# Kernel optimization log

Hardware: AMD Instinct MI355X
Metric: run time of the kernel (lower is better)

The kernel has to match this reference:

```python
import jax, jax.numpy as jnp
import numpy as np

T, B, I, H, O, L = 512, 64, 256, 1024, 256, 3


def _gru_layer(x_seq, h0, w_ih, w_hh, b_ih, b_hh):
    """PyTorch-style GRU layer. x_seq: [T,B,Iin], h0: [B,H].
    Gate order in stacked weights is (r, z, n), matching torch.nn.GRU."""
    # Precompute all input-side gate projections with one big GEMM: [T,B,3H]
    gi = jnp.einsum('tbi,gi->tbg', x_seq, w_ih) + b_ih

    def step(h, gi_t):
        gh = h @ w_hh.T + b_hh                      # [B,3H]
        i_r, i_z, i_n = jnp.split(gi_t, 3, axis=-1)
        h_r, h_z, h_n = jnp.split(gh, 3, axis=-1)
        r = jax.nn.sigmoid(i_r + h_r)
        z = jax.nn.sigmoid(i_z + h_z)
        n = jnp.tanh(i_n + r * h_n)
        h_new = (1.0 - z) * n + z * h
        return h_new, h_new

    h_last, ys = jax.lax.scan(step, h0, gi)
    return ys, h_last


def setup_inputs() -> dict:
    key = jax.random.key(0)
    ks = jax.random.split(key, 16)
    s = 1.0 / np.sqrt(H)  # torch init scale ~ U(-1/sqrt(H), 1/sqrt(H))
    inp = {
        'x': jax.random.normal(ks[0], (T, B, I), jnp.float32),
        'h0': jax.random.normal(ks[1], (L, B, H), jnp.float32),
        'fc_w': jax.random.uniform(ks[2], (O, H), jnp.float32, -s, s),
        'fc_b': jax.random.uniform(ks[3], (O,), jnp.float32, -s, s),
    }
    k_idx = 4
    for l in range(L):
        iin = I if l == 0 else H
        inp[f'w_ih_l{l}'] = jax.random.uniform(ks[k_idx], (3 * H, iin), jnp.float32, -s, s)
        inp[f'w_hh_l{l}'] = jax.random.uniform(ks[k_idx + 1], (3 * H, H), jnp.float32, -s, s)
        inp[f'b_ih_l{l}'] = jax.random.uniform(ks[k_idx + 2], (3 * H,), jnp.float32, -s, s)
        inp[f'b_hh_l{l}'] = jax.random.uniform(ks[k_idx + 3], (3 * H,), jnp.float32, -s, s)
        k_idx += 4
    return inp


def reference(x, h0,
              w_ih_l0, w_hh_l0, b_ih_l0, b_hh_l0,
              w_ih_l1, w_hh_l1, b_ih_l1, b_hh_l1,
              w_ih_l2, w_hh_l2, b_ih_l2, b_hh_l2,
              fc_w, fc_b):
    layer_params = [
        (w_ih_l0, w_hh_l0, b_ih_l0, b_hh_l0),
        (w_ih_l1, w_hh_l1, b_ih_l1, b_hh_l1),
        (w_ih_l2, w_hh_l2, b_ih_l2, b_hh_l2),
    ]
    out = x
    h_lasts = []
    for l, (wi, wh, bi, bh) in enumerate(layer_params):
        out, h_l = _gru_layer(out, h0[l], wi, wh, bi, bh)
        h_lasts.append(h_l)
    y = out @ fc_w.T + fc_b        # [T,B,O]
    h_final = jnp.stack(h_lasts)   # [L,B,H]
    return y, h_final
```

## Files before the change

### kernel.cpp

```cpp
#include <hip/hip_runtime.h>
#include <cstdint>
#include <cstddef>

#define TT 512
#define BB 64
#define II 256
#define HH 1024
#define OO 256
#define LL 3
#define NBLK 192
#define TSLOTS 513
#define SSTEPS 520
#define LDS_GI   98304
#define GI_STRIDE 68
#define LDS_HT   (LDS_GI + 26112)
#define LDS_TOTAL (LDS_HT + 2048)

typedef _Float16 half8 __attribute__((ext_vector_type(8)));
typedef float floatx4 __attribute__((ext_vector_type(4)));
typedef float float4v __attribute__((ext_vector_type(4)));

__device__ __forceinline__ floatx4 mfma16(half8 a, half8 b, floatx4 c) {
    return __builtin_amdgcn_mfma_f32_16x16x32_f16(a, b, c, 0, 0, 0);
}

__device__ __forceinline__ float fast_sig(float x) {
    return __builtin_amdgcn_rcpf(1.f + __builtin_amdgcn_exp2f(-1.44269504f * x));
}
__device__ __forceinline__ float fast_tanh(float x) {
    return 1.f - 2.f * __builtin_amdgcn_rcpf(1.f + __builtin_amdgcn_exp2f(2.88539008f * x));
}

__global__ void cast_f32_f16(const float* __restrict__ in, _Float16* __restrict__ out, int n) {
    int i = blockIdx.x * 256 + threadIdx.x;
    if (i < n) out[i] = (_Float16)in[i];
}

__global__ void init_h(const float* __restrict__ h0, _Float16* __restrict__ hseq,
                       unsigned* __restrict__ flags) {
    int i = blockIdx.x * 256 + threadIdx.x;
    if (i < 256) flags[i] = 0u;
    if (i >= LL * BB * HH) return;
    int l = i / (BB * HH);
    int rest = i - l * (BB * HH);
    hseq[((size_t)l * TSLOTS) * BB * HH + rest] = (_Float16)h0[i];
}

__global__ void frag_reorder(const float* __restrict__ src, _Float16* __restrict__ dst,
                             int K, int nks) {
    int idx = blockIdx.x * 256 + threadIdx.x;
    int total = 64 * 3 * nks * 64;
    if (idx >= total) return;
    int lane = idx & 63;
    int r = idx >> 6;
    int ks = r % nks; r /= nks;
    int g = r % 3;
    int jb = r / 3;
    int row = g * HH + jb * 16 + (lane & 15);
    int col = ks * 32 + (lane >> 4) * 8;
    const float* s8 = src + (size_t)row * K + col;
    half8 v;
#pragma unroll
    for (int i = 0; i < 8; ++i) v[i] = (_Float16)s8[i];
    *(half8*)(dst + (size_t)idx * 8) = v;
}

struct PArgs {
    const float* x;
    const float* h0;
    const _Float16* wih[3];
    const float* whh_src[3];
    const float* bih[3];
    const float* bhh[3];
    _Float16* hseq;
    float* out_h;
    unsigned* flags;
};

__global__ __launch_bounds__(512, 2) void gru_persistent(PArgs a) {
    extern __shared__ __align__(16) char lds[];
    float* giL = (float*)(lds + LDS_GI);
    _Float16* ht = (_Float16*)(lds + LDS_HT);
    const int layer = blockIdx.x >> 6;
    const int jb = blockIdx.x & 63;
    const int tid = threadIdx.x;
    const int lane = tid & 63;
    const int wv = tid >> 6;
    const bool isrec = wv < 4;
    const int lr = lane & 15, lq = lane >> 4;
    const int row0 = (wv & 3) << 4;
    const int j = (jb << 4) + lr;

    const int wih_nks = (layer == 0) ? 8 : 32;
    const _Float16* wih = a.wih[layer] + (size_t)jb * (size_t)(3 * wih_nks * 64 * 8)
                          + (size_t)lane * 8;

    {
        const float* wsrc = a.whh_src[layer];
        for (int c = tid; c < 6144; c += 512) {
            int lc = c & 63;
            int ks = (c >> 6) & 31;
            int g  = c >> 11;
            int row = g * HH + (jb << 4) + (lc & 15);
            int col = (ks << 5) + ((lc >> 4) << 3);
            const float* s8 = wsrc + (size_t)row * HH + col;
            half8 v;
#pragma unroll
            for (int i = 0; i < 8; ++i) v[i] = (_Float16)s8[i];
            *(half8*)(lds + (size_t)c * 16) = v;
        }
    }
    __syncthreads();

    const float bir = a.bih[layer][j], biz = a.bih[layer][HH + j], bin = a.bih[layer][2 * HH + j];
    const float bhr = a.bhh[layer][j], bhz = a.bhh[layer][HH + j], bhn = a.bhh[layer][2 * HH + j];
    const char* wb = lds + (size_t)lane * 16;

    float hprev[4];
    if (isrec) {
#pragma unroll
        for (int i2 = 0; i2 < 4; ++i2)
            hprev[i2] = a.h0[((size_t)layer * BB + row0 + lq * 4 + i2) * HH + j];
    }

    for (int s = 0; s < SSTEPS; ++s) {
        const int t  = s - (3 * layer + 2);
        const int tg = s - (3 * layer + 1);
        const bool t_valid = (t >= 0 && t < TT);
        const bool rec_act = isrec && t_valid;
        const bool gi_act = !isrec && tg >= 0 && tg < TT;

        if (rec_act) {
            for (;;) {
                unsigned f = __hip_atomic_load(&a.flags[layer * 64 + lane],
                                               __ATOMIC_RELAXED, __HIP_MEMORY_SCOPE_AGENT);
                if (__all(f >= (unsigned)s)) break;
                __builtin_amdgcn_s_sleep(2);
            }
            __builtin_amdgcn_sched_barrier(0);

            floatx4 ar{0.f,0.f,0.f,0.f}, az{0.f,0.f,0.f,0.f}, anh{0.f,0.f,0.f,0.f};
            const _Float16* Ah = a.hseq + ((size_t)layer * TSLOTS + t) * BB * HH
                                 + (size_t)(row0 + lr) * HH + lq * 8;
#pragma unroll
            for (int h2 = 0; h2 < 2; ++h2) {
                half8 av[16];
#pragma unroll
                for (int ks = 0; ks < 16; ++ks)
                    av[ks] = *(const half8*)(Ah + (h2 * 16 + ks) * 32);
#pragma unroll
                for (int ks = 0; ks < 16; ++ks) {
                    const int kk = h2 * 16 + ks;
                    ar  = mfma16(av[ks], *(const half8*)(wb + (0 * 32 + kk) * 1024), ar);
                    az  = mfma16(av[ks], *(const half8*)(wb + (1 * 32 + kk) * 1024), az);
                    anh = mfma16(av[ks], *(const half8*)(wb + (2 * 32 + kk) * 1024), anh);
                }
            }
            const int slot = t & 1;
#pragma unroll
            for (int i2 = 0; i2 < 4; ++i2) {
                int brow = row0 + lq * 4 + i2;
                float gir = giL[((slot * 3 + 0) * 16 + lr) * GI_STRIDE + brow];
                float giz = giL[((slot * 3 + 1) * 16 + lr) * GI_STRIDE + brow];
                float gin = giL[((slot * 3 + 2) * 16 + lr) * GI_STRIDE + brow];
                float rg = fast_sig(ar[i2] + gir + bir + bhr);
                float zg = fast_sig(az[i2] + giz + biz + bhz);
                float ng = fast_tanh(gin + bin + rg * (anh[i2] + bhn));
                float hnew = (1.f - zg) * ng + zg * hprev[i2];
                hprev[i2] = hnew;
                ht[brow * 16 + lr] = (_Float16)hnew;
                if (t == TT - 1) a.out_h[((size_t)layer * BB + brow) * HH + j] = hnew;
            }
        }
        if (gi_act) {
            const int slot = tg & 1;
            floatx4 g0{0.f,0.f,0.f,0.f}, g1{0.f,0.f,0.f,0.f}, g2{0.f,0.f,0.f,0.f};
            if (layer == 0) {
                const float* Ax = a.x + (size_t)tg * BB * II + (size_t)(row0 + lr) * II + lq * 8;
                float4v xa[16];
#pragma unroll
                for (int ks = 0; ks < 8; ++ks) {
                    xa[2 * ks]     = *(const float4v*)(Ax + ks * 32);
                    xa[2 * ks + 1] = *(const float4v*)(Ax + ks * 32 + 4);
                }
#pragma unroll
                for (int ks = 0; ks < 8; ++ks) {
                    half8 av;
#pragma unroll
                    for (int e = 0; e < 4; ++e) {
                        av[e]     = (_Float16)xa[2 * ks][e];
                        av[e + 4] = (_Float16)xa[2 * ks + 1][e];
                    }
                    g0 = mfma16(av, *(const half8*)(wih + (size_t)(0 * 8 + ks) * 512), g0);
                    g1 = mfma16(av, *(const half8*)(wih + (size_t)(1 * 8 + ks) * 512), g1);
                    g2 = mfma16(av, *(const half8*)(wih + (size_t)(2 * 8 + ks) * 512), g2);
                }
            } else {
                for (;;) {
                    unsigned f = __hip_atomic_load(&a.flags[(layer - 1) * 64 + lane],
                                                   __ATOMIC_RELAXED, __HIP_MEMORY_SCOPE_AGENT);
                    if (__all(f >= (unsigned)(s - 1))) break;
                    __builtin_amdgcn_s_sleep(2);
                }
                __builtin_amdgcn_sched_barrier(0);
                const _Float16* Ay = a.hseq + ((size_t)(layer - 1) * TSLOTS + (tg + 1)) * BB * HH
                                     + (size_t)(row0 + lr) * HH + lq * 8;
#pragma unroll
                for (int h2 = 0; h2 < 2; ++h2) {
                    half8 av[16];
#pragma unroll
                    for (int ks = 0; ks < 16; ++ks)
                        av[ks] = *(const half8*)(Ay + (h2 * 16 + ks) * 32);
#pragma unroll
                    for (int ks = 0; ks < 16; ++ks) {
                        const int kk = h2 * 16 + ks;
                        g0 = mfma16(av[ks], *(const half8*)(wih + (size_t)(0 * 32 + kk) * 512), g0);
                        g1 = mfma16(av[ks], *(const half8*)(wih + (size_t)(1 * 32 + kk) * 512), g1);
                        g2 = mfma16(av[ks], *(const half8*)(wih + (size_t)(2 * 32 + kk) * 512), g2);
                    }
                }
            }
#pragma unroll
            for (int q = 0; q < 4; ++q) {
                int brow = row0 + lq * 4 + q;
                giL[((slot * 3 + 0) * 16 + lr) * GI_STRIDE + brow] = g0[q];
                giL[((slot * 3 + 1) * 16 + lr) * GI_STRIDE + brow] = g1[q];
                giL[((slot * 3 + 2) * 16 + lr) * GI_STRIDE + brow] = g2[q];
            }
        }
        __syncthreads();

        if (t_valid && tid < 256) {
            int row = tid >> 2, cg = tid & 3;
            unsigned long long v = *(const unsigned long long*)(ht + row * 16 + cg * 4);
            _Float16* dst = a.hseq + ((size_t)layer * TSLOTS + (t + 1)) * BB * HH
                            + (size_t)row * HH + (jb << 4) + cg * 4;
            __hip_atomic_store((unsigned long long*)dst, v,
                               __ATOMIC_RELAXED, __HIP_MEMORY_SCOPE_AGENT);
        }
        __syncthreads();
        if (tid == 0)
            __hip_atomic_store(&a.flags[blockIdx.x], (unsigned)(s + 1),
                               __ATOMIC_RELAXED, __HIP_MEMORY_SCOPE_AGENT);
    }
}

__global__ __launch_bounds__(256) void fc_kernel(const _Float16* __restrict__ hseq,
                                                 const _Float16* __restrict__ w,
                                                 const float* __restrict__ bias,
                                                 float* __restrict__ out) {
    const int wid = (blockIdx.x << 2) + (threadIdx.x >> 6);
    const int lane = threadIdx.x & 63;
    const int mt = wid >> 1;
    const int no = (wid & 1) * 8;
    const int lr = lane & 15, lq = lane >> 4;
    const _Float16* Ar = hseq + ((size_t)2 * TSLOTS * BB + BB + (size_t)(mt * 16 + lr)) * HH
                         + lq * 8;
    floatx4 acc[8] = {};
    for (int k = 0; k < HH; k += 32) {
        half8 av = *(const half8*)(Ar + k);
#pragma unroll
        for (int i = 0; i < 8; ++i) {
            const _Float16* Br = w + (size_t)((no + i) * 16 + lr) * HH + lq * 8 + k;
            acc[i] = mfma16(av, *(const half8*)Br, acc[i]);
        }
    }
#pragma unroll
    for (int i = 0; i < 8; ++i) {
        float b = bias[(no + i) * 16 + lr];
#pragma unroll
        for (int q = 0; q < 4; ++q)
            out[(size_t)(mt * 16 + lq * 4 + q) * OO + (no + i) * 16 + lr] = acc[i][q] + b;
    }
}

extern "C" void kernel_launch(void* const* d_in, const int* in_sizes, int n_in,
                              void* d_out, int out_size, void* d_ws, size_t ws_size,
                              hipStream_t stream) {
    const float* x    = (const float*)d_in[0];
    const float* h0   = (const float*)d_in[1];
    const float* fc_w = (const float*)d_in[2];
    const float* fc_b = (const float*)d_in[3];
    const float* wih[3]; const float* whh[3]; const float* bih[3]; const float* bhh[3];
    for (int l = 0; l < 3; ++l) {
        wih[l] = (const float*)d_in[4 + l * 4 + 0];
        whh[l] = (const float*)d_in[4 + l * 4 + 1];
        bih[l] = (const float*)d_in[4 + l * 4 + 2];
        bhh[l] = (const float*)d_in[4 + l * 4 + 3];
    }

    char* p = (char*)d_ws;
    auto alloc = [&](size_t bytes) {
        char* q = p;
        p += (bytes + 255) & ~(size_t)255;
        return q;
    };
    _Float16* hseq = (_Float16*)alloc((size_t)LL * TSLOTS * BB * HH * 2);
    _Float16* wihf[3];
    wihf[0] = (_Float16*)alloc((size_t)3 * HH * II * 2);
    wihf[1] = (_Float16*)alloc((size_t)3 * HH * HH * 2);
    wihf[2] = (_Float16*)alloc((size_t)3 * HH * HH * 2);
    _Float16* fcw16 = (_Float16*)alloc((size_t)OO * HH * 2);
    unsigned* flags = (unsigned*)alloc(1024);
    if ((size_t)(p - (char*)d_ws) > ws_size) return;

    cast_f32_f16<<<(OO * HH + 255) / 256, 256, 0, stream>>>(fc_w, fcw16, OO * HH);
    frag_reorder<<<384, 256, 0, stream>>>(wih[0], wihf[0], II, 8);
    frag_reorder<<<1536, 256, 0, stream>>>(wih[1], wihf[1], HH, 32);
    frag_reorder<<<1536, 256, 0, stream>>>(wih[2], wihf[2], HH, 32);
    init_h<<<768, 256, 0, stream>>>(h0, hseq, flags);

    PArgs a;
    a.x = x;
    a.h0 = h0;
    for (int l = 0; l < 3; ++l) {
        a.wih[l] = wihf[l];
        a.whh_src[l] = whh[l];
        a.bih[l] = bih[l];
        a.bhh[l] = bhh[l];
    }
    a.hseq = hseq;
    a.out_h = (float*)d_out + (size_t)TT * BB * OO;
    a.flags = flags;

    hipFuncSetAttribute((const void*)gru_persistent,
                        hipFuncAttributeMaxDynamicSharedMemorySize, LDS_TOTAL);
    gru_persistent<<<NBLK, 512, LDS_TOTAL, stream>>>(a);

    fc_kernel<<<1024, 256, 0, stream>>>(hseq, fcw16, fc_b, (float*)d_out);
}
```

Baseline: 7.858 ms.

## Poll global flags from one wave and broadcast readiness via LDS mailbox

Only one wave per role (wave 0 for recurrent, wave 4 for input projection) now spins on the global step flags. It publishes the step number to an LDS mailbox that the other waves poll, which cuts global atomic polling traffic and shortens the sleep interval. The h loads are also issued all 32 at once instead of two halves of 16, and the gi reads from LDS are hoisted ahead of the MFMA loop to hide latency. The trade-offs are higher register pressure from 32 half8 operands and an added LDS hop in the signalling path.

```diff
diff --git a/kernel.cpp b/kernel.cpp
--- a/kernel.cpp
+++ b/kernel.cpp
@@ -14,7 +14,8 @@
 #define LDS_GI   98304
 #define GI_STRIDE 68
 #define LDS_HT   (LDS_GI + 26112)
-#define LDS_TOTAL (LDS_HT + 2048)
+#define LDS_MB   (LDS_HT + 2048)
+#define LDS_TOTAL (LDS_MB + 64)
 
 typedef _Float16 half8 __attribute__((ext_vector_type(8)));
 typedef float floatx4 __attribute__((ext_vector_type(4)));
@@ -81,6 +82,8 @@
     extern __shared__ __align__(16) char lds[];
     float* giL = (float*)(lds + LDS_GI);
     _Float16* ht = (_Float16*)(lds + LDS_HT);
+    volatile unsigned* ep_own  = (volatile unsigned*)(lds + LDS_MB);
+    volatile unsigned* ep_prev = (volatile unsigned*)(lds + LDS_MB + 4);
     const int layer = blockIdx.x >> 6;
     const int jb = blockIdx.x & 63;
     const int tid = threadIdx.x;
@@ -94,6 +97,8 @@
     const int wih_nks = (layer == 0) ? 8 : 32;
     const _Float16* wih = a.wih[layer] + (size_t)jb * (size_t)(3 * wih_nks * 64 * 8)
                           + (size_t)lane * 8;
+
+    if (tid == 0) { *ep_own = 0u; *ep_prev = 0u; }
 
     {
         const float* wsrc = a.whh_src[layer];
@@ -131,45 +136,56 @@
         const bool gi_act = !isrec && tg >= 0 && tg < TT;
 
         if (rec_act) {
-            for (;;) {
-                unsigned f = __hip_atomic_load(&a.flags[layer * 64 + lane],
-                                               __ATOMIC_RELAXED, __HIP_MEMORY_SCOPE_AGENT);
-                if (__all(f >= (unsigned)s)) break;
-                __builtin_amdgcn_s_sleep(2);
+            if (wv == 0) {
+                for (;;) {
+                    unsigned f = __hip_atomic_load(&a.flags[layer * 64 + lane],
+                                                   __ATOMIC_RELAXED, __HIP_MEMORY_SCOPE_AGENT);
+                    if (__all(f >= (unsigned)s)) break;
+                    __builtin_amdgcn_s_sleep(1);
+                }
+                if (lane == 0) *ep_own = (unsigned)s;
+            } else {
+                while (*ep_own < (unsigned)s) __builtin_amdgcn_s_sleep(1);
             }
             __builtin_amdgcn_sched_barrier(0);
 
-            floatx4 ar{0.f,0.f,0.f,0.f}, az{0.f,0.f,0.f,0.f}, anh{0.f,0.f,0.f,0.f};
+            const int slot = t & 1;
+            float gir[4], giz[4], gin[4];
+#pragma unroll
+            for (int i2 = 0; i2 < 4; ++i2) {
+                int brow = row0 + lq * 4 + i2;
+                gir[i2] = giL[((slot * 3 + 0) * 16 + lr) * GI_STRIDE + brow];
+                giz[i2] = giL[((slot * 3 + 1) * 16 + lr) * GI_STRIDE + brow];
+                gin[i2] = giL[((slot * 3 + 2) * 16 + lr) * GI_STRIDE + brow];
+            }
+
             const _Float16* Ah = a.hseq + ((size_t)layer * TSLOTS + t) * BB * HH
                                  + (size_t)(row0 + lr) * HH + lq * 8;
-#pragma unroll
-            for (int h2 = 0; h2 < 2; ++h2) {
-                half8 av[16];
-#pragma unroll
-                for (int ks = 0; ks < 16; ++ks)
-                    av[ks] = *(const half8*)(Ah + (h2 * 16 + ks) * 32);
-#pragma unroll
-                for (int ks = 0; ks < 16; ++ks) {
-                    const int kk = h2 * 16 + ks;
-                    ar  = mfma16(av[ks], *(const half8*)(wb + (0 * 32 + kk) * 1024), ar);
-                    az  = mfma16(av[ks], *(const half8*)(wb + (1 * 32 + kk) * 1024), az);
-                    anh = mfma16(av[ks], *(const half8*)(wb + (2 * 32 + kk) * 1024), anh);
-                }
-            }
-            const int slot = t & 1;
+            half8 av[32];
+#pragma unroll
+            for (int ks = 0; ks < 32; ++ks)
+                av[ks] = *(const half8*)(Ah + ks * 32);
+            floatx4 ar{0.f,0.f,0.f,0.f}, az{0.f,0.f,0.f,0.f}, anh{0.f,0.f,0.f,0.f};
+#pragma unroll
+            for (int ks = 0; ks < 32; ++ks) {
+                ar  = mfma16(av[ks], *(const half8*)(wb + (0 * 32 + ks) * 1024), ar);
+                az  = mfma16(av[ks], *(const half8*)(wb + (1 * 32 + ks) * 1024), az);
+                anh = mfma16(av[ks], *(const half8*)(wb + (2 * 32 + ks) * 1024), anh);
+            }
 #pragma unroll
             for (int i2 = 0; i2 < 4; ++i2) {
                 int brow = row0 + lq * 4 + i2;
-                float gir = giL[((slot * 3 + 0) * 16 + lr) * GI_STRIDE + brow];
-                float giz = giL[((slot * 3 + 1) * 16 + lr) * GI_STRIDE + brow];
-                float gin = giL[((slot * 3 + 2) * 16 + lr) * GI_STRIDE + brow];
-                float rg = fast_sig(ar[i2] + gir + bir + bhr);
-                float zg = fast_sig(az[i2] + giz + biz + bhz);
-                float ng = fast_tanh(gin + bin + rg * (anh[i2] + bhn));
+                float rg = fast_sig(ar[i2] + gir[i2] + bir + bhr);
+                float zg = fast_sig(az[i2] + giz[i2] + biz + bhz);
+                float ng = fast_tanh(gin[i2] + bin + rg * (anh[i2] + bhn));
                 float hnew = (1.f - zg) * ng + zg * hprev[i2];
                 hprev[i2] = hnew;
                 ht[brow * 16 + lr] = (_Float16)hnew;
-                if (t == TT - 1) a.out_h[((size_t)layer * BB + brow) * HH + j] = hnew;
+            }
+            if (t == TT - 1) {
+#pragma unroll
+                for (int i2 = 0; i2 < 4; ++i2)
+                    a.out_h[((size_t)layer * BB + row0 + lq * 4 + i2) * HH + j] = hprev[i2];
             }
         }
         if (gi_act) {
@@ -196,28 +212,29 @@
                     g2 = mfma16(av, *(const half8*)(wih + (size_t)(2 * 8 + ks) * 512), g2);
                 }
             } else {
-                for (;;) {
-                    unsigned f = __hip_atomic_load(&a.flags[(layer - 1) * 64 + lane],
-                                                   __ATOMIC_RELAXED, __HIP_MEMORY_SCOPE_AGENT);
-                    if (__all(f >= (unsigned)(s - 1))) break;
-                    __builtin_amdgcn_s_sleep(2);
+                if (wv == 4) {
+                    for (;;) {
+                        unsigned f = __hip_atomic_load(&a.flags[(layer - 1) * 64 + lane],
+                                                       __ATOMIC_RELAXED, __HIP_MEMORY_SCOPE_AGENT);
+                        if (__all(f >= (unsigned)(s - 1))) break;
+                        __builtin_amdgcn_s_sleep(1);
+                    }
+                    if (lane == 0) *ep_prev = (unsigned)s;
+                } else {
+                    while (*ep_prev < (unsigned)s) __builtin_amdgcn_s_sleep(1);
                 }
                 __builtin_amdgcn_sched_barrier(0);
                 const _Float16* Ay = a.hseq + ((size_t)(layer - 1) * TSLOTS + (tg + 1)) * BB * HH
                                      + (size_t)(row0 + lr) * HH + lq * 8;
-#pragma unroll
-                for (int h2 = 0; h2 < 2; ++h2) {
-                    half8 av[16];
-#pragma unroll
-                    for (int ks = 0; ks < 16; ++ks)
-                        av[ks] = *(const half8*)(Ay + (h2 * 16 + ks) * 32);
-#pragma unroll
-                    for (int ks = 0; ks < 16; ++ks) {
-                        const int kk = h2 * 16 + ks;
-                        g0 = mfma16(av[ks], *(const half8*)(wih + (size_t)(0 * 32 + kk) * 512), g0);
-                        g1 = mfma16(av[ks], *(const half8*)(wih + (size_t)(1 * 32 + kk) * 512), g1);
-                        g2 = mfma16(av[ks], *(const half8*)(wih + (size_t)(2 * 32 + kk) * 512), g2);
-                    }
+                half8 av[32];
+#pragma unroll
+                for (int ks = 0; ks < 32; ++ks)
+                    av[ks] = *(const half8*)(Ay + ks * 32);
+#pragma unroll
+                for (int ks = 0; ks < 32; ++ks) {
+                    g0 = mfma16(av[ks], *(const half8*)(wih + (size_t)(0 * 32 + ks) * 512), g0);
+                    g1 = mfma16(av[ks], *(const half8*)(wih + (size_t)(1 * 32 + ks) * 512), g1);
+                    g2 = mfma16(av[ks], *(const half8*)(wih + (size_t)(2 * 32 + ks) * 512), g2);
                 }
             }
 #pragma unroll
```

Result: faster. 7.333 ms (-6.7%).
